# Kernel tuning notes

Measured on AMD Instinct MI355X. Metric: run time of the kernel, lower is better.

## Reference

```python
import jax, jax.numpy as jnp
import numpy as np

B, D, H = 4096, 1024, 1024


def setup_inputs() -> dict:
    key = jax.random.key(0)
    ks = jax.random.split(key, 20)
    s_in = 1.0 / np.sqrt(D)
    s_hid = 1.0 / np.sqrt(H)
    inp = {
        "x_t": jax.random.normal(ks[0], (B, D), dtype=jnp.float32),
        "h_t_1": jax.random.normal(ks[1], (B, H), dtype=jnp.float32),
        "c_t_1": jax.random.normal(ks[2], (B, H), dtype=jnp.float32),
        # input-to-hidden weights (nn.Linear: y = x @ W.T + b), stacked i,f,o,z
        "W": jax.random.uniform(ks[3], (4, H, D), minval=-s_in, maxval=s_in, dtype=jnp.float32),
        "bW": jax.random.uniform(ks[4], (4, H), minval=-s_in, maxval=s_in, dtype=jnp.float32),
        # hidden-to-hidden weights, stacked i,f,o,z
        "U": jax.random.uniform(ks[5], (4, H, H), minval=-s_hid, maxval=s_hid, dtype=jnp.float32),
        "bU": jax.random.uniform(ks[6], (4, H), minval=-s_hid, maxval=s_hid, dtype=jnp.float32),
    }
    return inp


def reference(x_t, h_t_1, c_t_1, W, bW, U, bU):
    # Two stacked GEMMs: [B,D]x[4,H,D] -> [4,B,H], [B,H]x[4,H,H] -> [4,B,H]
    gx = jnp.einsum("bd,ghd->gbh", x_t, W) + bW[:, None, :]
    gh = jnp.einsum("bh,gkh->gbk", h_t_1, U) + bU[:, None, :]
    g = gx + gh  # [4, B, H] pre-activations for i, f, o, z
    i = jax.nn.sigmoid(g[0])
    f = jax.nn.sigmoid(g[1])
    o = jax.nn.sigmoid(g[2])
    z = jnp.tanh(g[3])
    c_t = i * z + f * c_t_1
    h_t = o * jnp.tanh(c_t)
    return (h_t, c_t)
```

## Files before the change

kernel.cpp:

```cpp
#include <hip/hip_runtime.h>
#include <math.h>

#define Mm 4096
#define Nn 4096
#define Kk 2048

typedef __bf16 bf16x8 __attribute__((ext_vector_type(8)));
typedef float f32x4 __attribute__((ext_vector_type(4)));

__device__ __forceinline__ unsigned short f2bf(float f) {
    union { float f; unsigned u; } v; v.f = f;
    unsigned r = v.u + 0x7FFFu + ((v.u >> 16) & 1u);
    return (unsigned short)(r >> 16);
}
__device__ __forceinline__ float bf2f(unsigned short s) {
    union { unsigned u; float f; } v; v.u = ((unsigned)s) << 16;
    return v.f;
}

__global__ void pack_bf16(const float* __restrict__ x, const float* __restrict__ h,
                          const float* __restrict__ W, const float* __restrict__ U,
                          unsigned short* __restrict__ Xc, unsigned short* __restrict__ Wc) {
    const int PER = (4096 * 1024) / 4;
    for (int t = blockIdx.x * blockDim.x + threadIdx.x; t < 4 * PER;
         t += gridDim.x * blockDim.x) {
        int region = t >> 20;
        int i = t & (PER - 1);
        int row = i >> 8;
        int c4  = i & 255;
        const float* src = (region == 0) ? x : (region == 1) ? h : (region == 2) ? W : U;
        unsigned short* dst = (region < 2) ? Xc : Wc;
        int koff = (region & 1) << 10;
        float4 v = reinterpret_cast<const float4*>(src)[i];
        ushort4 o;
        o.x = f2bf(v.x); o.y = f2bf(v.y); o.z = f2bf(v.z); o.w = f2bf(v.w);
        *reinterpret_cast<ushort4*>(dst + (size_t)row * 2048 + koff + c4 * 4) = o;
    }
}

__device__ __forceinline__ void gl16(const void* g, void* l) {
    __builtin_amdgcn_global_load_lds(
        (const __attribute__((address_space(1))) void*)g,
        (__attribute__((address_space(3))) void*)l, 16, 0, 0);
}

#define A_OFF(p, ah) (((p) * 2 + (ah)) * 16384)
#define B_OFF(p, hb) (65536 + ((p) * 2 + (hb)) * 16384)

__global__ __launch_bounds__(512, 2) void gemm_8ph(const unsigned short* __restrict__ A,
                                                   const unsigned short* __restrict__ Bw,
                                                   unsigned short* __restrict__ Cg) {
    extern __shared__ char lds[];
    const int tid = threadIdx.x, lane = tid & 63, wave = tid >> 6;
    const int wm = wave >> 2, wn = wave & 3;

    const int bid = blockIdx.x;
    const int swz = (bid & 7) * 32 + (bid >> 3);
    const int bm = swz & 15, bn = swz >> 4;
    const size_t Crow0 = (size_t)bm * 256, Ccol0 = (size_t)bn * 256;

    const int srow = wave * 8 + (lane >> 3);
    const int scolswz = (((lane & 7) ^ (lane >> 3)) << 4);
    const char* aS[2][2];
    const char* bS[2][2];
#pragma unroll
    for (int ah = 0; ah < 2; ++ah)
#pragma unroll
        for (int j = 0; j < 2; ++j) {
            aS[ah][j] = (const char*)A  + (size_t)(Crow0 + ah * 128 + j * 64 + srow) * 4096 + scolswz;
            bS[ah][j] = (const char*)Bw + (size_t)(Ccol0 + ah * 128 + j * 64 + srow) * 4096 + scolswz;
        }

#define STG_A(p, ah, kb) do { \
        gl16(aS[ah][0] + (kb), lds + A_OFF(p, ah) + wave * 1024); \
        gl16(aS[ah][1] + (kb), lds + A_OFF(p, ah) + 8192 + wave * 1024); } while (0)
#define STG_B(p, hb, kb) do { \
        gl16(bS[hb][0] + (kb), lds + B_OFF(p, hb) + wave * 1024); \
        gl16(bS[hb][1] + (kb), lds + B_OFF(p, hb) + 8192 + wave * 1024); } while (0)

    const int arowB = (wm * 64 + (lane & 15)) * 128;
    const int browB = ((wn & 1) * 64 + (lane & 15)) * 128;
    const int c0 = (((lane >> 4) << 4)) ^ ((lane & 7) << 4);
    const int c1 = (64 + ((lane >> 4) << 4)) ^ ((lane & 7) << 4);
    const int bhb = wn >> 1;

#define LDA(p, ah, mfl, ck) (*(const bf16x8*)(lds + A_OFF(p, ah) + arowB + (mfl) * 2048 + (ck)))
#define LDB(p, nf, ck)      (*(const bf16x8*)(lds + B_OFF(p, bhb) + browB + (nf) * 2048 + (ck)))

    f32x4 acc[2][4][4] = {};

#define MF8(ah, mf, ak0, ak1) \
    acc[ah][mf][0] = __builtin_amdgcn_mfma_f32_16x16x32_bf16(ak0, b00, acc[ah][mf][0], 0, 0, 0); \
    acc[ah][mf][0] = __builtin_amdgcn_mfma_f32_16x16x32_bf16(ak1, b01, acc[ah][mf][0], 0, 0, 0); \
    acc[ah][mf][1] = __builtin_amdgcn_mfma_f32_16x16x32_bf16(ak0, b10, acc[ah][mf][1], 0, 0, 0); \
    acc[ah][mf][1] = __builtin_amdgcn_mfma_f32_16x16x32_bf16(ak1, b11, acc[ah][mf][1], 0, 0, 0); \
    acc[ah][mf][2] = __builtin_amdgcn_mfma_f32_16x16x32_bf16(ak0, b20, acc[ah][mf][2], 0, 0, 0); \
    acc[ah][mf][2] = __builtin_amdgcn_mfma_f32_16x16x32_bf16(ak1, b21, acc[ah][mf][2], 0, 0, 0); \
    acc[ah][mf][3] = __builtin_amdgcn_mfma_f32_16x16x32_bf16(ak0, b30, acc[ah][mf][3], 0, 0, 0); \
    acc[ah][mf][3] = __builtin_amdgcn_mfma_f32_16x16x32_bf16(ak1, b31, acc[ah][mf][3], 0, 0, 0);

#define PH_TAIL \
    __builtin_amdgcn_s_barrier(); \
    asm volatile("s_waitcnt lgkmcnt(0)" ::: "memory"); \
    __builtin_amdgcn_s_setprio(1);

#define PH_END \
    __builtin_amdgcn_s_setprio(0); \
    __builtin_amdgcn_s_barrier();

#define GROUP(p, kbA1, kbT2) \
    { \
        bf16x8 b00 = LDB(p, 0, c0), b01 = LDB(p, 0, c1), b10 = LDB(p, 1, c0), b11 = LDB(p, 1, c1); \
        bf16x8 b20 = LDB(p, 2, c0), b21 = LDB(p, 2, c1), b30 = LDB(p, 3, c0), b31 = LDB(p, 3, c1); \
        {  \
            bf16x8 a00 = LDA(p, 0, 0, c0), a01 = LDA(p, 0, 0, c1); \
            bf16x8 a10 = LDA(p, 0, 1, c0), a11 = LDA(p, 0, 1, c1); \
            STG_A((p) ^ 1, 1, kbA1); \
            PH_TAIL MF8(0, 0, a00, a01) MF8(0, 1, a10, a11) PH_END \
        } \
        {  \
            bf16x8 a00 = LDA(p, 0, 2, c0), a01 = LDA(p, 0, 2, c1); \
            bf16x8 a10 = LDA(p, 0, 3, c0), a11 = LDA(p, 0, 3, c1); \
            STG_B(p, 0, kbT2); \
            PH_TAIL MF8(0, 2, a00, a01) MF8(0, 3, a10, a11) PH_END \
        } \
        {  \
            bf16x8 a00 = LDA(p, 1, 0, c0), a01 = LDA(p, 1, 0, c1); \
            bf16x8 a10 = LDA(p, 1, 1, c0), a11 = LDA(p, 1, 1, c1); \
            STG_A(p, 0, kbT2); \
            PH_TAIL MF8(1, 0, a00, a01) MF8(1, 1, a10, a11) PH_END \
        } \
        {  \
            bf16x8 a00 = LDA(p, 1, 2, c0), a01 = LDA(p, 1, 2, c1); \
            bf16x8 a10 = LDA(p, 1, 3, c0), a11 = LDA(p, 1, 3, c1); \
            STG_B(p, 1, kbT2); \
            __builtin_amdgcn_s_barrier(); \
            asm volatile("s_waitcnt lgkmcnt(0)" ::: "memory"); \
            __builtin_amdgcn_s_setprio(1); \
            MF8(1, 2, a00, a01) MF8(1, 3, a10, a11) \
            __builtin_amdgcn_s_setprio(0); \
            asm volatile("s_waitcnt vmcnt(6)" ::: "memory"); \
            __builtin_amdgcn_s_barrier(); \
        } \
    }

    STG_B(0, 0, 0);
    STG_A(0, 0, 0);
    STG_B(0, 1, 0);
    STG_A(0, 1, 0);
    STG_B(1, 0, 128);
    STG_A(1, 0, 128);
    STG_B(1, 1, 128);
    asm volatile("s_waitcnt vmcnt(6)" ::: "memory");
    __builtin_amdgcn_s_barrier();

    for (int it = 0; it < 16; ++it) {
        const int t0 = 2 * it;
        const size_t kA1_0 = (size_t)(t0 + 1) * 128;
        const size_t kT2_0 = (t0 + 2 <= 31) ? (size_t)(t0 + 2) * 128 : 0;
        const size_t kA1_1 = kT2_0;
        const size_t kT2_1 = (t0 + 3 <= 31) ? (size_t)(t0 + 3) * 128 : 0;
        GROUP(0, kA1_0, kT2_0)
        GROUP(1, kA1_1, kT2_1)
    }

    const int er0 = (lane >> 4) * 4;
    const int ec = lane & 15;
#pragma unroll
    for (int ah = 0; ah < 2; ++ah)
#pragma unroll
        for (int mf = 0; mf < 4; ++mf)
#pragma unroll
            for (int r = 0; r < 4; ++r) {
                const size_t row = Crow0 + ah * 128 + wm * 64 + mf * 16 + er0 + r;
#pragma unroll
                for (int nf = 0; nf < 4; ++nf) {
                    const size_t col = Ccol0 + wn * 64 + nf * 16 + ec;
                    Cg[row * 4096 + col] = f2bf(acc[ah][mf][nf][r]);
                }
            }
}

__global__ void lstm_elt(const unsigned short* __restrict__ g,
                         const float* __restrict__ cprev,
                         const float* __restrict__ bW, const float* __restrict__ bU,
                         float* __restrict__ out) {
    int t = blockIdx.x * blockDim.x + threadIdx.x;
    int b = t >> 10, h = t & 1023;
    const unsigned short* gb = g + ((size_t)b << 12);
    float gi = bf2f(gb[h])        + bW[h]        + bU[h];
    float gf = bf2f(gb[1024 + h]) + bW[1024 + h] + bU[1024 + h];
    float go = bf2f(gb[2048 + h]) + bW[2048 + h] + bU[2048 + h];
    float gz = bf2f(gb[3072 + h]) + bW[3072 + h] + bU[3072 + h];
    float iv = 1.f / (1.f + __expf(-gi));
    float fv = 1.f / (1.f + __expf(-gf));
    float ov = 1.f / (1.f + __expf(-go));
    float zv = tanhf(gz);
    float cv = fmaf(iv, zv, fv * cprev[t]);
    float hv = ov * tanhf(cv);
    out[t] = hv;
    out[(1 << 22) + t] = cv;
}

extern "C" void kernel_launch(void* const* d_in, const int* in_sizes, int n_in,
                              void* d_out, int out_size, void* d_ws, size_t ws_size,
                              hipStream_t stream) {
    const float* x  = (const float*)d_in[0];
    const float* h  = (const float*)d_in[1];
    const float* c  = (const float*)d_in[2];
    const float* W  = (const float*)d_in[3];
    const float* bW = (const float*)d_in[4];
    const float* U  = (const float*)d_in[5];
    const float* bU = (const float*)d_in[6];
    float* out = (float*)d_out;

    char* ws = (char*)d_ws;
    unsigned short* Xc = (unsigned short*)ws;
    unsigned short* Wc = (unsigned short*)(ws + ((size_t)16 << 20));
    unsigned short* Gp = (unsigned short*)(ws + ((size_t)32 << 20));

    (void)hipFuncSetAttribute((const void*)gemm_8ph,
                              hipFuncAttributeMaxDynamicSharedMemorySize, 131072);

    hipLaunchKernelGGL(pack_bf16, dim3(2048), dim3(256), 0, stream, x, h, W, U, Xc, Wc);
    hipLaunchKernelGGL(gemm_8ph, dim3(256), dim3(512), 131072, stream, Xc, Wc, Gp);
    hipLaunchKernelGGL(lstm_elt, dim3((4096 * 1024) / 256), dim3(256), 0, stream,
                       Gp, c, bW, bU, out);
}
```

Before: 95.68 us.

## Fuse LSTM gate epilogue into GEMM via interleaved weight layout

Reorders the packed weight rows so the four gates of each hidden unit sit in adjacent output columns, then computes the LSTM cell update directly in the GEMM epilogue. Accumulators are staged through LDS with a swizzle so each lane reads its four gate values as one vector. Bias sums are precomputed once in the pack kernel. This drops the bf16 gate intermediate write/read and the separate elementwise kernel launch, and also avoids rounding the gate values to bf16, at the cost of extra barriers and LDS traffic in the epilogue.

```diff
diff --git a/kernel.cpp b/kernel.cpp
--- a/kernel.cpp
+++ b/kernel.cpp
@@ -13,14 +13,20 @@
     unsigned r = v.u + 0x7FFFu + ((v.u >> 16) & 1u);
     return (unsigned short)(r >> 16);
 }
-__device__ __forceinline__ float bf2f(unsigned short s) {
-    union { unsigned u; float f; } v; v.u = ((unsigned)s) << 16;
-    return v.f;
-}
 
 __global__ void pack_bf16(const float* __restrict__ x, const float* __restrict__ h,
                           const float* __restrict__ W, const float* __restrict__ U,
-                          unsigned short* __restrict__ Xc, unsigned short* __restrict__ Wc) {
+                          const float* __restrict__ bW, const float* __restrict__ bU,
+                          unsigned short* __restrict__ Xc, unsigned short* __restrict__ Wc,
+                          float* __restrict__ bsum) {
+    if (blockIdx.x == 0) {
+#pragma unroll
+        for (int j = 0; j < 16; ++j) {
+            int n = threadIdx.x * 16 + j;
+            int hh = n >> 2, g = n & 3;
+            bsum[n] = bW[g * 1024 + hh] + bU[g * 1024 + hh];
+        }
+    }
     const int PER = (4096 * 1024) / 4;
     for (int t = blockIdx.x * blockDim.x + threadIdx.x; t < 4 * PER;
          t += gridDim.x * blockDim.x) {
@@ -29,12 +35,15 @@
         int row = i >> 8;
         int c4  = i & 255;
         const float* src = (region == 0) ? x : (region == 1) ? h : (region == 2) ? W : U;
-        unsigned short* dst = (region < 2) ? Xc : Wc;
-        int koff = (region & 1) << 10;
         float4 v = reinterpret_cast<const float4*>(src)[i];
         ushort4 o;
         o.x = f2bf(v.x); o.y = f2bf(v.y); o.z = f2bf(v.z); o.w = f2bf(v.w);
-        *reinterpret_cast<ushort4*>(dst + (size_t)row * 2048 + koff + c4 * 4) = o;
+        if (region < 2) {
+            *reinterpret_cast<ushort4*>(Xc + (size_t)row * 2048 + (region << 10) + c4 * 4) = o;
+        } else {
+            int g = row >> 10, hh = row & 1023;
+            *reinterpret_cast<ushort4*>(Wc + (size_t)(hh * 4 + g) * 2048 + ((region & 1) << 10) + c4 * 4) = o;
+        }
     }
 }
 
@@ -49,7 +58,9 @@
 
 __global__ __launch_bounds__(512, 2) void gemm_8ph(const unsigned short* __restrict__ A,
                                                    const unsigned short* __restrict__ Bw,
-                                                   unsigned short* __restrict__ Cg) {
+                                                   const float* __restrict__ bsum,
+                                                   const float* __restrict__ cprev,
+                                                   float* __restrict__ out) {
     extern __shared__ char lds[];
     const int tid = threadIdx.x, lane = tid & 63, wave = tid >> 6;
     const int wm = wave >> 2, wn = wave & 3;
@@ -164,42 +175,48 @@
         GROUP(1, kA1_1, kT2_1)
     }
 
-    const int er0 = (lane >> 4) * 4;
-    const int ec = lane & 15;
-#pragma unroll
-    for (int ah = 0; ah < 2; ++ah)
+    __syncthreads();
+
+    const int Hbase = (int)(Ccol0 >> 2);
+    const int ec = lane & 15, er0 = (lane >> 4) * 4;
+
+#pragma unroll
+    for (int ah = 0; ah < 2; ++ah) {
+        if (ah) __syncthreads();
 #pragma unroll
         for (int mf = 0; mf < 4; ++mf)
 #pragma unroll
             for (int r = 0; r < 4; ++r) {
-                const size_t row = Crow0 + ah * 128 + wm * 64 + mf * 16 + er0 + r;
+                const int lrow = wm * 64 + mf * 16 + er0 + r;
+                const int sw = (lrow & 4) << 4;
 #pragma unroll
                 for (int nf = 0; nf < 4; ++nf) {
-                    const size_t col = Ccol0 + wn * 64 + nf * 16 + ec;
-                    Cg[row * 4096 + col] = f2bf(acc[ah][mf][nf][r]);
+                    const int col = wn * 64 + nf * 16 + ec;
+                    *(float*)(lds + lrow * 1024 + ((col * 4) ^ sw)) = acc[ah][mf][nf][r];
                 }
             }
-}
-
-__global__ void lstm_elt(const unsigned short* __restrict__ g,
-                         const float* __restrict__ cprev,
-                         const float* __restrict__ bW, const float* __restrict__ bU,
-                         float* __restrict__ out) {
-    int t = blockIdx.x * blockDim.x + threadIdx.x;
-    int b = t >> 10, h = t & 1023;
-    const unsigned short* gb = g + ((size_t)b << 12);
-    float gi = bf2f(gb[h])        + bW[h]        + bU[h];
-    float gf = bf2f(gb[1024 + h]) + bW[1024 + h] + bU[1024 + h];
-    float go = bf2f(gb[2048 + h]) + bW[2048 + h] + bU[2048 + h];
-    float gz = bf2f(gb[3072 + h]) + bW[3072 + h] + bU[3072 + h];
-    float iv = 1.f / (1.f + __expf(-gi));
-    float fv = 1.f / (1.f + __expf(-gf));
-    float ov = 1.f / (1.f + __expf(-go));
-    float zv = tanhf(gz);
-    float cv = fmaf(iv, zv, fv * cprev[t]);
-    float hv = ov * tanhf(cv);
-    out[t] = hv;
-    out[(1 << 22) + t] = cv;
+        __syncthreads();
+#pragma unroll
+        for (int i = 0; i < 16; ++i) {
+            const int lrow = i * 8 + wave;
+            const int sw = (lrow & 4) << 4;
+            f32x4 g4 = *(const f32x4*)(lds + lrow * 1024 + ((lane * 16) ^ sw));
+            f32x4 bs = *(const f32x4*)(bsum + (size_t)(Hbase + lane) * 4);
+            const size_t bg = Crow0 + ah * 128 + lrow;
+            const size_t oidx = bg * 1024 + Hbase + lane;
+            float cp = cprev[oidx];
+            float gi = g4[0] + bs[0], gf = g4[1] + bs[1];
+            float go = g4[2] + bs[2], gz = g4[3] + bs[3];
+            float iv = 1.f / (1.f + __expf(-gi));
+            float fv = 1.f / (1.f + __expf(-gf));
+            float ov = 1.f / (1.f + __expf(-go));
+            float zv = tanhf(gz);
+            float cc = fmaf(iv, zv, fv * cp);
+            float hv = ov * tanhf(cc);
+            out[oidx] = hv;
+            out[(1 << 22) + oidx] = cc;
+        }
+    }
 }
 
 extern "C" void kernel_launch(void* const* d_in, const int* in_sizes, int n_in,
@@ -217,13 +234,13 @@
     char* ws = (char*)d_ws;
     unsigned short* Xc = (unsigned short*)ws;
     unsigned short* Wc = (unsigned short*)(ws + ((size_t)16 << 20));
-    unsigned short* Gp = (unsigned short*)(ws + ((size_t)32 << 20));
+    float* bsum = (float*)(ws + ((size_t)32 << 20));
 
     (void)hipFuncSetAttribute((const void*)gemm_8ph,
                               hipFuncAttributeMaxDynamicSharedMemorySize, 131072);
 
-    hipLaunchKernelGGL(pack_bf16, dim3(2048), dim3(256), 0, stream, x, h, W, U, Xc, Wc);
-    hipLaunchKernelGGL(gemm_8ph, dim3(256), dim3(512), 131072, stream, Xc, Wc, Gp);
-    hipLaunchKernelGGL(lstm_elt, dim3((4096 * 1024) / 256), dim3(256), 0, stream,
-                       Gp, c, bW, bU, out);
-}
+    hipLaunchKernelGGL(pack_bf16, dim3(2048), dim3(256), 0, stream,
+                       x, h, W, U, bW, bU, Xc, Wc, bsum);
+    hipLaunchKernelGGL(gemm_8ph, dim3(256), dim3(512), 131072, stream,
+                       Xc, Wc, bsum, c, out);
+}
```

New measurement: 87.68 us. -8.4%, faster.
